# Optimization experiments

Measured on AMD Instinct MI355X. Metric: run time of the kernel, lower is better.

The kernel has to match this reference:

```python
import jax, jax.numpy as jnp
from jax import lax
import numpy as np

N, T, I, H = 128, 2048, 128, 1024


def setup_inputs() -> dict:
    key = jax.random.key(0)
    k1, k2, k3, k4, k5 = jax.random.split(key, 5)
    return {
        "x": jax.random.normal(k1, (N, T, I), dtype=jnp.float32),
        "w_ih": jax.random.normal(k2, (H, I), dtype=jnp.float32) * (1.0 / np.sqrt(I)),
        "b_ih": jax.random.normal(k3, (H,), dtype=jnp.float32) * 0.01,
        "w_hh": jax.random.normal(k4, (H, H), dtype=jnp.float32) * (1.0 / np.sqrt(H)),
        "initial": jax.random.normal(k5, (N, H), dtype=jnp.float32),
    }


def reference(x, w_ih, b_ih, w_hh, initial):
    # Precompute input projection for all timesteps at once: [N, T, H]
    proj = jnp.einsum("nti,hi->nth", x, w_ih) + b_ih
    # First hidden: initial noise + W_ih x_0
    h0 = initial + proj[:, 0]  # [N, H]
    # Steps t=1..T-1 use x[:, t-1] (faithful to the original off-by-one):
    # time-major projections for indices 0..T-2 -> [T-1, N, H]
    xs = jnp.swapaxes(proj[:, :-1], 0, 1)

    def step(h, p):
        h_new = h @ w_hh.T + p  # purely linear recurrence
        return h_new, h_new

    _, hs = lax.scan(step, h0, xs)  # hs: [T-1, N, H]
    hidden_tensor = jnp.concatenate([h0[None], hs], axis=0)  # [T, N, H]
    hidden_tensor = jnp.transpose(hidden_tensor, (1, 0, 2))  # [N, T, H]
    return (hidden_tensor, hidden_tensor)
```

## Files before the change

### kernel.cpp

```cpp
#include <hip/hip_runtime.h>
#include <stdint.h>

typedef unsigned int u32;
typedef unsigned short u16;
typedef _Float16 f16;
typedef __attribute__((ext_vector_type(4))) float f32x4;
typedef __attribute__((ext_vector_type(8))) short s16x8;
typedef __attribute__((ext_vector_type(8))) _Float16 f16x8;

#define NB 128
#define TS 2048
#define ID 128
#define HD 1024
#define LCH 16
#define CCH 128
#define NJT 64

__device__ __forceinline__ u16 f2bf(float f) {
  u32 u = __builtin_bit_cast(u32, f);
  u += 0x7FFFu + ((u >> 16) & 1u);
  return (u16)(u >> 16);
}
__device__ __forceinline__ float bf2f(u16 h) {
  u32 u = ((u32)h) << 16;
  return __builtin_bit_cast(float, u);
}
__device__ __forceinline__ void split2(float f, u16& hi, u16& lo) {
  hi = f2bf(f);
  lo = f2bf(f - bf2f(hi));
}
__device__ __forceinline__ float ntl(const float* p) { return __builtin_nontemporal_load(p); }
__device__ __forceinline__ f32x4 ntl4(const float* p) {
  return __builtin_nontemporal_load((const f32x4*)p);
}
__device__ __forceinline__ void nts(float v, float* p) { __builtin_nontemporal_store(v, p); }
__device__ __forceinline__ void nts4(f32x4 v, float* p) {
  __builtin_nontemporal_store(v, (f32x4*)p);
}
#define MFMA16(a, b, c) __builtin_amdgcn_mfma_f32_16x16x32_bf16((a), (b), (c), 0, 0, 0)
#define MFMAH(a, b, c) __builtin_amdgcn_mfma_f32_16x16x32_f16((a), (b), (c), 0, 0, 0)


__global__ void k_pack_b(const float* __restrict__ src, long sk, long sj, int jtiles,
                         int total, u16* __restrict__ dh, u16* __restrict__ dl) {
  const int fid = blockIdx.x * blockDim.x + threadIdx.x;
  if (fid >= total) return;
  const int lane = fid & 63;
  const int tt = fid >> 6;
  const int jt = tt % jtiles;
  const int kt = tt / jtiles;
  const int k0 = kt * 32 + (lane >> 4) * 8;
  const long j = jt * 16 + (lane & 15);
  s16x8 hv, lv;
#pragma unroll
  for (int i = 0; i < 8; ++i) {
    const float v = src[(long)(k0 + i) * sk + j * sj];
    u16 hh, ll; split2(v, hh, ll);
    hv[i] = (short)hh; lv[i] = (short)ll;
  }
  *(s16x8*)(dh + (long)fid * 8) = hv;
  *(s16x8*)(dl + (long)fid * 8) = lv;
}

__global__ void k_pack_f16(const float* __restrict__ src, long sk, long sj, int jtiles,
                           int total, u16* __restrict__ dh) {
  const int fid = blockIdx.x * blockDim.x + threadIdx.x;
  if (fid >= total) return;
  const int lane = fid & 63;
  const int tt = fid >> 6;
  const int jt = tt % jtiles;
  const int kt = tt / jtiles;
  const int k0 = kt * 32 + (lane >> 4) * 8;
  const long j = jt * 16 + (lane & 15);
  s16x8 hv;
#pragma unroll
  for (int i = 0; i < 8; ++i) {
    const float v = src[(long)(k0 + i) * sk + j * sj];
    const f16 hh = (f16)v;
    hv[i] = (short)__builtin_bit_cast(u16, hh);
  }
  *(s16x8*)(dh + (long)fid * 8) = hv;
}

__global__ void k_split_strided(const float* __restrict__ src, long sk, long sj, int nj,
                                long total, u16* __restrict__ dh, u16* __restrict__ dl) {
  const long i = (long)blockIdx.x * blockDim.x + threadIdx.x;
  if (i >= total) return;
  const long k = i / nj;
  const long j = i % nj;
  u16 hh, ll;
  split2(src[k * sk + j * sj], hh, ll);
  dh[i] = hh;
  dl[i] = ll;
}

__global__ void k_copy(const float* __restrict__ s, float* __restrict__ d, long n4) {
  const long i0 = (long)blockIdx.x * blockDim.x + threadIdx.x;
  const long stride = (long)gridDim.x * blockDim.x;
  for (long i = i0; i < n4; i += stride) {
    const f32x4 v = __builtin_nontemporal_load((const f32x4*)s + i);
    __builtin_nontemporal_store(v, (f32x4*)d + i);
  }
}

template <int EPI, int RT, int CT, int ASRC>
__global__ __launch_bounds__(256) void k_gemm3(
    const u16* __restrict__ ahi, const u16* __restrict__ alo,
    const float* __restrict__ af32, long lda,
    const u16* __restrict__ bhi, const u16* __restrict__ blo, int ksteps,
    const float* __restrict__ aux, float* __restrict__ cout, long ldc,
    u16* __restrict__ drm_h, u16* __restrict__ drm_l,
    u16* __restrict__ dpk_h, u16* __restrict__ dpk_l,
    u16* __restrict__ zb16, u32* __restrict__ zmx,
    const u16* __restrict__ einh, const u16* __restrict__ einl, int ksd) {
  __shared__ float cb[4][16][33];
  const int tid = threadIdx.x;
  const int l = tid & 63;
  const int w = tid >> 6;
  const int wr = w >> 1, wc = w & 1;
  const int n0 = blockIdx.y * (32 * CT) + wc * (16 * CT);
  if constexpr (EPI == 4) {
    if ((int)blockIdx.x < ksd) {
      const long rbase = (long)blockIdx.x * (32 * RT);
      const int ncols8 = (32 * CT) / 8;
      const int nb0 = blockIdx.y * (32 * CT);
      for (int i = tid; i < (32 * RT) * ncols8; i += 256) {
        const int rr = i / ncols8;
        const int cc = (i % ncols8) * 8;
        const long o = (rbase + rr) * HD + nb0 + cc;
        *(s16x8*)(drm_h + o) = *(const s16x8*)(einh + o);
        *(s16x8*)(drm_l + o) = *(const s16x8*)(einl + o);
      }
      return;
    }
  }
  const long m0 = ((long)blockIdx.x - ((EPI == 4) ? ksd : 0)) * (32 * RT) + wr * (16 * RT);
  const int arow = l & 15, koff = (l >> 4) * 8;
  f32x4 acc[RT][CT];
#pragma unroll
  for (int a = 0; a < RT; ++a)
#pragma unroll
    for (int b = 0; b < CT; ++b) acc[a][b] = (f32x4){0.f, 0.f, 0.f, 0.f};
#pragma unroll 1
  for (int ks = 0; ks < ksteps; ++ks) {
    s16x8 AH[RT], AL[RT], BH[CT], BL[CT];
#pragma unroll
    for (int rt = 0; rt < RT; ++rt) {
      const long off = (m0 + rt * 16 + arow) * lda + ks * 32 + koff;
      if constexpr (ASRC == 0) {
        AH[rt] = *(const s16x8*)(ahi + off);
        AL[rt] = *(const s16x8*)(alo + off);
      } else {
        const float4 f0 = *(const float4*)(af32 + off);
        const float4 f1 = *(const float4*)(af32 + off + 4);
        float fv[8] = {f0.x, f0.y, f0.z, f0.w, f1.x, f1.y, f1.z, f1.w};
        s16x8 hv, lv;
#pragma unroll
        for (int i = 0; i < 8; ++i) {
          u16 hh, ll; split2(fv[i], hh, ll);
          hv[i] = (short)hh; lv[i] = (short)ll;
        }
        AH[rt] = hv; AL[rt] = lv;
      }
    }
#pragma unroll
    for (int ct = 0; ct < CT; ++ct) {
      const long off = (((long)ks * NJT + (n0 >> 4) + ct) * 64 + l) * 8;
      BH[ct] = *(const s16x8*)(bhi + off);
      BL[ct] = *(const s16x8*)(blo + off);
    }
#pragma unroll
    for (int ct = 0; ct < CT; ++ct)
#pragma unroll
      for (int rt = 0; rt < RT; ++rt) {
        acc[rt][ct] = MFMA16(AH[rt], BH[ct], acc[rt][ct]);
        acc[rt][ct] = MFMA16(AL[rt], BH[ct], acc[rt][ct]);
        acc[rt][ct] = MFMA16(AH[rt], BL[ct], acc[rt][ct]);
      }
  }
  const int crow = (l >> 4) * 4, ccol = l & 15;
  if constexpr (EPI == 1) {
#pragma unroll
    for (int rt = 0; rt < RT; ++rt)
#pragma unroll
      for (int ctp = 0; ctp < CT / 2; ++ctp) {
#pragma unroll
        for (int e = 0; e < 2; ++e)
#pragma unroll
          for (int r = 0; r < 4; ++r)
            cb[w][crow + r][e * 16 + ccol] = acc[rt][2 * ctp + e][r];
        const int rr = l >> 2, c8 = (l & 3) * 8;
        const int colg = n0 + ctp * 32 + c8;
        const float4 b0 = *(const float4*)&aux[colg];
        const float4 b1 = *(const float4*)&aux[colg + 4];
        f32x4 v0, v1;
        v0[0] = cb[w][rr][c8 + 0] + b0.x; v0[1] = cb[w][rr][c8 + 1] + b0.y;
        v0[2] = cb[w][rr][c8 + 2] + b0.z; v0[3] = cb[w][rr][c8 + 3] + b0.w;
        v1[0] = cb[w][rr][c8 + 4] + b1.x; v1[1] = cb[w][rr][c8 + 5] + b1.y;
        v1[2] = cb[w][rr][c8 + 6] + b1.z; v1[3] = cb[w][rr][c8 + 7] + b1.w;
        const long row = m0 + rt * 16 + rr;
        nts4(v0, cout + row * ldc + colg);
        nts4(v1, cout + row * ldc + colg + 4);
      }
  } else if constexpr (EPI == 2) {
    float mym = 0.f;
#pragma unroll
    for (int rt = 0; rt < RT; ++rt)
#pragma unroll
      for (int ct = 0; ct < CT; ++ct) {
        const int col = n0 + ct * 16 + ccol;
#pragma unroll
        for (int r = 0; r < 4; ++r) {
          const long row = m0 + rt * 16 + crow + r;
          const int slot = (int)(row >> 7);
          const int n = (int)(row & 127);
          const float z = acc[rt][ct][r] +
              aux[((long)n * TS + (long)(slot + 1) * LCH - 1) * HD + col];
          zb16[((long)slot * NB + n) * HD + col] = f2bf(z);
          mym = fmaxf(mym, fabsf(z));
        }
      }
#pragma unroll
    for (int d = 1; d < 64; d <<= 1) mym = fmaxf(mym, __shfl_xor(mym, d));
    if (l == 0) {
      const int slot = (int)(m0 >> 7);
      atomicMax(&zmx[slot + 1], __builtin_bit_cast(u32, mym));
    }
  } else if constexpr (EPI == 4) {
    const long rshift = (long)ksd * (32 * RT);
#pragma unroll
    for (int rt = 0; rt < RT; ++rt)
#pragma unroll
      for (int ct = 0; ct < CT; ++ct) {
        const int col = n0 + ct * 16 + ccol;
#pragma unroll
        for (int r = 0; r < 4; ++r) {
          const long row = m0 + rt * 16 + crow + r;
          const long o = (row + rshift) * HD + col;
          const float v = acc[rt][ct][r] + bf2f(einh[o]) + bf2f(einl[o]);
          u16 hh, ll; split2(v, hh, ll);
          drm_h[o] = hh;
          drm_l[o] = ll;
        }
      }
  } else {
#pragma unroll
    for (int rt = 0; rt < RT; ++rt)
#pragma unroll
      for (int ct = 0; ct < CT; ++ct) {
        const int col = n0 + ct * 16 + ccol;
#pragma unroll
        for (int r = 0; r < 4; ++r) {
          const long row = m0 + rt * 16 + crow + r;
          const float v = acc[rt][ct][r];
          u16 hh, ll; split2(v, hh, ll);
          drm_h[row * HD + col] = hh;
          drm_l[row * HD + col] = ll;
          const int lane2 = ((((int)row >> 3) & 3) << 4) | (col & 15);
          const long poff = (((row >> 5) * NJT + (col >> 4)) * 64 + lane2) * 8 + (row & 7);
          dpk_h[poff] = hh;
          dpk_l[poff] = ll;
        }
      }
  }
}

template <int EMIT>
__global__ __launch_bounds__(1024, 4) __attribute__((amdgpu_waves_per_eu(4, 4)))
void k_scan2(
    const float* __restrict__ proj, const float* __restrict__ initial,
    const u16* __restrict__ wph,
    const u16* __restrict__ zbuf, const u32* __restrict__ zmx,
    u16* __restrict__ ebh, u16* __restrict__ ebl, float* __restrict__ out1) {
  __shared__ u16 st[64 * HD];
  const int b = blockIdx.x;
  const int c = b >> 1;
  const int g = b & 1;
  const int tid = threadIdx.x;
  const int l = tid & 63;
  const int w = tid >> 6;
  const long t0 = (long)c * LCH;
  const int ccol = l & 15;
  const int q = l >> 4;
  const int jt0 = w * 4;
  const int akey = l & 15;

  float s = 1.f, inv_s = 1.f;
  if constexpr (EMIT) {
    const u32 zb = zmx[c];
    const int ex = (int)((zb >> 23) & 255u) - 127;
    const int k = ex > 8 ? ex - 8 : 0;
    s = __builtin_bit_cast(float, (u32)(127 + k) << 23);
    inv_s = __builtin_bit_cast(float, (u32)(127 - k) << 23);
  }

  for (int i = tid; i < 64 * HD; i += 1024) {
    const int r = i >> 10;
    const int col = i & (HD - 1);
    const int n = g * 64 + r;
    float v;
    if (c == 0) {
      v = ntl(initial + (long)n * HD + col) + ntl(proj + ((long)n * TS) * HD + col);
    } else {
      if constexpr (EMIT) v = bf2f(zbuf[((long)(c - 1) * NB + n) * HD + col]);
      else                v = ntl(proj + ((long)n * TS + t0 - 1) * HD + col);
    }
    const f16 hv = (f16)(v * inv_s);
    const int si = r * HD + ((((col >> 3) ^ (r & 15)) << 3) | (col & 7));
    st[si] = __builtin_bit_cast(u16, hv);
    if constexpr (EMIT) {
      nts(v, out1 + ((long)n * TS + t0) * HD + col);
    }
  }
  __syncthreads();

#pragma unroll 1
  for (int step = 1; step < LCH; ++step) {
    const long t = t0 + step;
    f32x4 acc[4][4];
#pragma unroll
    for (int rt = 0; rt < 4; ++rt)
#pragma unroll
      for (int ct = 0; ct < 4; ++ct) acc[rt][ct] = (f32x4){0.f, 0.f, 0.f, 0.f};
    __builtin_amdgcn_s_setprio(1);
#pragma unroll 2
    for (int ks = 0; ks < 32; ++ks) {
      const int colpart = ((((ks << 2) | q) ^ akey) << 3);
      const f16x8 a0 = __builtin_bit_cast(f16x8, *(const s16x8*)&st[(0 * 16 + ccol) * HD + colpart]);
      const f16x8 a1 = __builtin_bit_cast(f16x8, *(const s16x8*)&st[(1 * 16 + ccol) * HD + colpart]);
      const f16x8 a2 = __builtin_bit_cast(f16x8, *(const s16x8*)&st[(2 * 16 + ccol) * HD + colpart]);
      const f16x8 a3 = __builtin_bit_cast(f16x8, *(const s16x8*)&st[(3 * 16 + ccol) * HD + colpart]);
#pragma unroll
      for (int ct = 0; ct < 4; ++ct) {
        const long boff = (((long)ks * NJT + jt0 + ct) * 64 + l) * 8;
        const f16x8 bh = __builtin_bit_cast(f16x8, *(const s16x8*)(wph + boff));
        acc[0][ct] = MFMAH(a0, bh, acc[0][ct]);
        acc[1][ct] = MFMAH(a1, bh, acc[1][ct]);
        acc[2][ct] = MFMAH(a2, bh, acc[2][ct]);
        acc[3][ct] = MFMAH(a3, bh, acc[3][ct]);
      }
    }
    __builtin_amdgcn_s_setprio(0);
    __syncthreads();
#pragma unroll
    for (int rt = 0; rt < 4; ++rt)
#pragma unroll
      for (int ct = 0; ct < 4; ++ct) {
        const int colb = (jt0 + ct) * 16 + ccol;
        const int cb7 = colb & 7;
        const int cblk = colb >> 3;
#pragma unroll
        for (int r = 0; r < 4; ++r) {
          const int row = rt * 16 + q * 4 + r;
          const f16 hv = (f16)acc[rt][ct][r];
          const int si = row * HD + (((cblk ^ (row & 15)) << 3) | cb7);
          st[si] = __builtin_bit_cast(u16, hv);
        }
      }
    __syncthreads();
#pragma unroll
    for (int it = 0; it < 8; ++it) {
      const int idx = tid + it * 1024;
      const int r = idx >> 7;
      const int cb8 = (idx & 127) << 3;
      const int n = g * 64 + r;
      const int si = r * HD + (((cb8 >> 3) ^ (r & 15)) << 3);
      const s16x8 av = *(const s16x8*)&st[si];
      const f32x4 p0 = ntl4(proj + ((long)n * TS + t - 1) * HD + cb8);
      const f32x4 p1 = ntl4(proj + ((long)n * TS + t - 1) * HD + cb8 + 4);
      float v[8];
      v[0] = (float)__builtin_bit_cast(f16, (u16)av[0]) + p0[0] * inv_s;
      v[1] = (float)__builtin_bit_cast(f16, (u16)av[1]) + p0[1] * inv_s;
      v[2] = (float)__builtin_bit_cast(f16, (u16)av[2]) + p0[2] * inv_s;
      v[3] = (float)__builtin_bit_cast(f16, (u16)av[3]) + p0[3] * inv_s;
      v[4] = (float)__builtin_bit_cast(f16, (u16)av[4]) + p1[0] * inv_s;
      v[5] = (float)__builtin_bit_cast(f16, (u16)av[5]) + p1[1] * inv_s;
      v[6] = (float)__builtin_bit_cast(f16, (u16)av[6]) + p1[2] * inv_s;
      v[7] = (float)__builtin_bit_cast(f16, (u16)av[7]) + p1[3] * inv_s;
      s16x8 nv;
#pragma unroll
      for (int j2 = 0; j2 < 8; ++j2)
        nv[j2] = (short)__builtin_bit_cast(u16, (f16)v[j2]);
      *(s16x8*)&st[si] = nv;
      if constexpr (EMIT) {
        f32x4 o0, o1;
        o0[0] = v[0] * s; o0[1] = v[1] * s; o0[2] = v[2] * s; o0[3] = v[3] * s;
        o1[0] = v[4] * s; o1[1] = v[5] * s; o1[2] = v[6] * s; o1[3] = v[7] * s;
        const long o = ((long)n * TS + t) * HD + cb8;
        nts4(o0, out1 + o);
        nts4(o1, out1 + o + 4);
      }
    }
    __syncthreads();
  }
  if constexpr (!EMIT) {
    for (int i = tid; i < 64 * HD; i += 1024) {
      const int r = i >> 10;
      const int col = i & (HD - 1);
      const int si = r * HD + ((((col >> 3) ^ (r & 15)) << 3) | (col & 7));
      const float v = (float)__builtin_bit_cast(f16, st[si]);
      u16 hh, ll; split2(v, hh, ll);
      const long o = ((long)c * NB + g * 64 + r) * HD + col;
      ebh[o] = hh;
      ebl[o] = ll;
    }
  }
}


extern "C" void kernel_launch(void* const* d_in, const int* in_sizes, int n_in,
                              void* d_out, int out_size, void* d_ws, size_t ws_size,
                              hipStream_t stream) {
  const float* x = (const float*)d_in[0];
  const float* w_ih = (const float*)d_in[1];
  const float* b_ih = (const float*)d_in[2];
  const float* w_hh = (const float*)d_in[3];
  const float* initial = (const float*)d_in[4];

  char* r1 = (char*)d_out;
  float* out1 = (float*)d_out;
  float* proj = out1 + (long)NB * TS * HD;
  float* out2 = proj;

  u16* xph = (u16*)(r1 + 0L);
  u16* xpl = (u16*)(r1 + 33554432L);
  u16* xqh = (u16*)(r1 + 67108864L);
  u16* xql = (u16*)(r1 + 100663296L);
  u16* wt_pk_h = (u16*)(r1 + 134217728L);
  u16* wt_pk_l = (u16*)(r1 + 136314880L);
  u16* wt_rm_h = (u16*)(r1 + 138412032L);
  u16* wt_rm_l = (u16*)(r1 + 140509184L);
  u16* rm_pp_h[2] = {(u16*)(r1 + 142606336L), (u16*)(r1 + 146800640L)};
  u16* rm_pp_l[2] = {(u16*)(r1 + 144703488L), (u16*)(r1 + 148897792L)};
  u16* pk_pp_h[2] = {(u16*)(r1 + 150994944L), (u16*)(r1 + 155189248L)};
  u16* pk_pp_l[2] = {(u16*)(r1 + 153092096L), (u16*)(r1 + 157286400L)};
  u16* wih_h = (u16*)(r1 + 159383552L);
  u16* wih_l = (u16*)(r1 + 159645696L);
  u16* wp_pk_h[7];
  u16* wp_pk_l[7];
  for (int j = 0; j < 7; ++j) {
    wp_pk_h[j] = (u16*)(r1 + 161480704L + (long)j * 4194304L);
    wp_pk_l[j] = (u16*)(r1 + 161480704L + (long)j * 4194304L + 2097152L);
  }

  char* wsb = (char*)d_ws;
  u16* wt16_h = (u16*)(wsb + 0L);
  u16* zbuf = (u16*)(wsb + 4194304L);
  u32* zmx = (u32*)(wsb + 37486592L);

  (void)hipMemsetAsync(zmx, 0, 512, stream);

  k_pack_b<<<512, 256, 0, stream>>>(w_hh, 1L, (long)HD, NJT, 32 * NJT * 64, wt_pk_h, wt_pk_l);
  k_pack_f16<<<512, 256, 0, stream>>>(w_hh, 1L, (long)HD, NJT, 32 * NJT * 64, wt16_h);
  k_pack_b<<<64, 256, 0, stream>>>(w_ih, 1L, (long)ID, NJT, 4 * NJT * 64, wih_h, wih_l);
  k_split_strided<<<4096, 256, 0, stream>>>(w_hh, 1L, (long)HD, HD, (long)HD * HD, wt_rm_h, wt_rm_l);

  dim3 gproj(2048, 8);
  k_gemm3<1, 4, 4, 1><<<gproj, 256, 0, stream>>>(
      nullptr, nullptr, x, (long)ID, wih_h, wih_l, ID / 32,
      b_ih, proj, (long)HD, nullptr, nullptr, nullptr, nullptr,
      nullptr, nullptr, nullptr, nullptr, 0);

  const u16 *arh = wt_rm_h, *arl = wt_rm_l, *aph = wt_pk_h, *apl = wt_pk_l;
  dim3 g1616(16, 16);
  for (int i = 0; i < 10; ++i) {
    u16* orh = rm_pp_h[i & 1];
    u16* orl = rm_pp_l[i & 1];
    u16* oph = (i >= 3) ? wp_pk_h[i - 3] : pk_pp_h[i & 1];
    u16* opl = (i >= 3) ? wp_pk_l[i - 3] : pk_pp_l[i & 1];
    k_gemm3<3, 2, 2, 0><<<g1616, 256, 0, stream>>>(
        arh, arl, nullptr, (long)HD, aph, apl, HD / 32,
        nullptr, nullptr, 0L, orh, orl, oph, opl,
        nullptr, nullptr, nullptr, nullptr, 0);
    arh = orh; arl = orl; aph = oph; apl = opl;
  }

  k_scan2<0><<<256, 1024, 0, stream>>>(proj, initial, wt16_h,
                                       nullptr, nullptr, xph, xpl, nullptr);

  const u16 *xin_h = xph, *xin_l = xpl;
  u16 *xout_h = xqh, *xout_l = xql;
  for (int j = 0; j < 7; ++j) {
    const int d = 1 << j;
    dim3 gks(CCH, 8);
    k_gemm3<4, 4, 4, 0><<<gks, 256, 0, stream>>>(
        xin_h, xin_l, nullptr, (long)HD, wp_pk_h[j], wp_pk_l[j], HD / 32,
        nullptr, nullptr, 0L, xout_h, xout_l,
        nullptr, nullptr, nullptr, nullptr, xin_h, xin_l, d);
    const u16* th = xin_h; const u16* tl = xin_l;
    xin_h = xout_h; xin_l = xout_l;
    xout_h = (u16*)th; xout_l = (u16*)tl;
  }

  dim3 gz(127, 8);
  k_gemm3<2, 4, 4, 0><<<gz, 256, 0, stream>>>(
      xin_h, xin_l, nullptr, (long)HD, wt_pk_h, wt_pk_l, HD / 32,
      proj, nullptr, 0L, nullptr, nullptr, nullptr, nullptr,
      zbuf, zmx, nullptr, nullptr, 0);

  k_scan2<1><<<256, 1024, 0, stream>>>(proj, initial, wt16_h,
                                       zbuf, zmx, nullptr, nullptr, out1);

  k_copy<<<2048, 256, 0, stream>>>(out1, out2, (long)NB * TS * HD / 4);
}
```

Before: 5.078 ms.

## Drop final copy kernel by dual-writing scan output and shifting projection storage

Removes the trailing full-size copy of the hidden tensor into the second output. The scan now writes every result to both outputs directly. Because the second output buffer also holds the projection, the projection GEMM now stores each row shifted by one timestep, with t=0 duplicated. That way the scan reads projS at index t and overwrites it in place with the same row. This saves one full read of the 1 GiB output but doubles scan store traffic and relies on in-place read-before-write ordering within each block.

```diff
diff --git a/kernel.cpp b/kernel.cpp
--- a/kernel.cpp
+++ b/kernel.cpp
@@ -92,15 +92,6 @@
   split2(src[k * sk + j * sj], hh, ll);
   dh[i] = hh;
   dl[i] = ll;
-}
-
-__global__ void k_copy(const float* __restrict__ s, float* __restrict__ d, long n4) {
-  const long i0 = (long)blockIdx.x * blockDim.x + threadIdx.x;
-  const long stride = (long)gridDim.x * blockDim.x;
-  for (long i = i0; i < n4; i += stride) {
-    const f32x4 v = __builtin_nontemporal_load((const f32x4*)s + i);
-    __builtin_nontemporal_store(v, (f32x4*)d + i);
-  }
 }
 
 template <int EPI, int RT, int CT, int ASRC>
@@ -199,8 +190,15 @@
         v1[0] = cb[w][rr][c8 + 4] + b1.x; v1[1] = cb[w][rr][c8 + 5] + b1.y;
         v1[2] = cb[w][rr][c8 + 6] + b1.z; v1[3] = cb[w][rr][c8 + 7] + b1.w;
         const long row = m0 + rt * 16 + rr;
-        nts4(v0, cout + row * ldc + colg);
-        nts4(v1, cout + row * ldc + colg + 4);
+        const int t = (int)(row & (TS - 1));
+        if (t != TS - 1) {
+          nts4(v0, cout + (row + 1) * ldc + colg);
+          nts4(v1, cout + (row + 1) * ldc + colg + 4);
+        }
+        if (t == 0) {
+          nts4(v0, cout + row * ldc + colg);
+          nts4(v1, cout + row * ldc + colg + 4);
+        }
       }
   } else if constexpr (EPI == 2) {
     float mym = 0.f;
@@ -215,7 +213,7 @@
           const int slot = (int)(row >> 7);
           const int n = (int)(row & 127);
           const float z = acc[rt][ct][r] +
-              aux[((long)n * TS + (long)(slot + 1) * LCH - 1) * HD + col];
+              aux[((long)n * TS + (long)(slot + 1) * LCH) * HD + col];
           zb16[((long)slot * NB + n) * HD + col] = f2bf(z);
           mym = fmaxf(mym, fabsf(z));
         }
@@ -268,10 +266,11 @@
 template <int EMIT>
 __global__ __launch_bounds__(1024, 4) __attribute__((amdgpu_waves_per_eu(4, 4)))
 void k_scan2(
-    const float* __restrict__ proj, const float* __restrict__ initial,
+    const float* __restrict__ projS, const float* __restrict__ initial,
     const u16* __restrict__ wph,
     const u16* __restrict__ zbuf, const u32* __restrict__ zmx,
-    u16* __restrict__ ebh, u16* __restrict__ ebl, float* __restrict__ out1) {
+    u16* __restrict__ ebh, u16* __restrict__ ebl,
+    float* __restrict__ out1, float* __restrict__ out2) {
   __shared__ u16 st[64 * HD];
   const int b = blockIdx.x;
   const int c = b >> 1;
@@ -300,16 +299,18 @@
     const int n = g * 64 + r;
     float v;
     if (c == 0) {
-      v = ntl(initial + (long)n * HD + col) + ntl(proj + ((long)n * TS) * HD + col);
+      v = ntl(initial + (long)n * HD + col) + ntl(projS + ((long)n * TS) * HD + col);
     } else {
       if constexpr (EMIT) v = bf2f(zbuf[((long)(c - 1) * NB + n) * HD + col]);
-      else                v = ntl(proj + ((long)n * TS + t0 - 1) * HD + col);
+      else                v = ntl(projS + ((long)n * TS + t0) * HD + col);
     }
     const f16 hv = (f16)(v * inv_s);
     const int si = r * HD + ((((col >> 3) ^ (r & 15)) << 3) | (col & 7));
     st[si] = __builtin_bit_cast(u16, hv);
     if constexpr (EMIT) {
-      nts(v, out1 + ((long)n * TS + t0) * HD + col);
+      const long o = ((long)n * TS + t0) * HD + col;
+      nts(v, out1 + o);
+      nts(v, out2 + o);
     }
   }
   __syncthreads();
@@ -366,8 +367,9 @@
       const int n = g * 64 + r;
       const int si = r * HD + (((cb8 >> 3) ^ (r & 15)) << 3);
       const s16x8 av = *(const s16x8*)&st[si];
-      const f32x4 p0 = ntl4(proj + ((long)n * TS + t - 1) * HD + cb8);
-      const f32x4 p1 = ntl4(proj + ((long)n * TS + t - 1) * HD + cb8 + 4);
+      const long po = ((long)n * TS + t) * HD + cb8;
+      const f32x4 p0 = ntl4(projS + po);
+      const f32x4 p1 = ntl4(projS + po + 4);
       float v[8];
       v[0] = (float)__builtin_bit_cast(f16, (u16)av[0]) + p0[0] * inv_s;
       v[1] = (float)__builtin_bit_cast(f16, (u16)av[1]) + p0[1] * inv_s;
@@ -386,9 +388,10 @@
         f32x4 o0, o1;
         o0[0] = v[0] * s; o0[1] = v[1] * s; o0[2] = v[2] * s; o0[3] = v[3] * s;
         o1[0] = v[4] * s; o1[1] = v[5] * s; o1[2] = v[6] * s; o1[3] = v[7] * s;
-        const long o = ((long)n * TS + t) * HD + cb8;
-        nts4(o0, out1 + o);
-        nts4(o1, out1 + o + 4);
+        nts4(o0, out1 + po);
+        nts4(o1, out1 + po + 4);
+        nts4(o0, out2 + po);
+        nts4(o1, out2 + po + 4);
       }
     }
     __syncthreads();
@@ -419,8 +422,8 @@
 
   char* r1 = (char*)d_out;
   float* out1 = (float*)d_out;
-  float* proj = out1 + (long)NB * TS * HD;
-  float* out2 = proj;
+  float* projS = out1 + (long)NB * TS * HD;
+  float* out2 = projS;
 
   u16* xph = (u16*)(r1 + 0L);
   u16* xpl = (u16*)(r1 + 33554432L);
@@ -458,7 +461,7 @@
   dim3 gproj(2048, 8);
   k_gemm3<1, 4, 4, 1><<<gproj, 256, 0, stream>>>(
       nullptr, nullptr, x, (long)ID, wih_h, wih_l, ID / 32,
-      b_ih, proj, (long)HD, nullptr, nullptr, nullptr, nullptr,
+      b_ih, projS, (long)HD, nullptr, nullptr, nullptr, nullptr,
       nullptr, nullptr, nullptr, nullptr, 0);
 
   const u16 *arh = wt_rm_h, *arl = wt_rm_l, *aph = wt_pk_h, *apl = wt_pk_l;
@@ -475,8 +478,8 @@
     arh = orh; arl = orl; aph = oph; apl = opl;
   }
 
-  k_scan2<0><<<256, 1024, 0, stream>>>(proj, initial, wt16_h,
-                                       nullptr, nullptr, xph, xpl, nullptr);
+  k_scan2<0><<<256, 1024, 0, stream>>>(projS, initial, wt16_h,
+                                       nullptr, nullptr, xph, xpl, nullptr, nullptr);
 
   const u16 *xin_h = xph, *xin_l = xpl;
   u16 *xout_h = xqh, *xout_l = xql;
@@ -495,11 +498,9 @@
   dim3 gz(127, 8);
   k_gemm3<2, 4, 4, 0><<<gz, 256, 0, stream>>>(
       xin_h, xin_l, nullptr, (long)HD, wt_pk_h, wt_pk_l, HD / 32,
-      proj, nullptr, 0L, nullptr, nullptr, nullptr, nullptr,
+      projS, nullptr, 0L, nullptr, nullptr, nullptr, nullptr,
       zbuf, zmx, nullptr, nullptr, 0);
 
-  k_scan2<1><<<256, 1024, 0, stream>>>(proj, initial, wt16_h,
-                                       zbuf, zmx, nullptr, nullptr, out1);
-
-  k_copy<<<2048, 256, 0, stream>>>(out1, out2, (long)NB * TS * HD / 4);
-}
+  k_scan2<1><<<256, 1024, 0, stream>>>(projS, initial, wt16_h,
+                                       zbuf, zmx, nullptr, nullptr, out1, out2);
+}
```

After: 4.801 ms. 5.4% less time.
